# Optimization experiments

Hardware: AMD Instinct MI355X
Metric: run time of the kernel (lower is better)

The kernel has to match this reference:

```python
import jax, jax.numpy as jnp
import numpy as np

DIM = 1024
HEADS = 16
HEAD_DIM = DIM // HEADS
WINDOW = 512
NEG = -1e9  # matches masked_fill(-1e9) semantics; excluded keys get ~0 weight


def setup_inputs() -> dict:
    key = jax.random.key(0)
    ks = jax.random.split(key, 9)
    s = 1.0 / np.sqrt(DIM)
    inp = {"x": jax.random.normal(ks[0], (2, 4096, DIM), dtype=jnp.float32)}
    for i, name in enumerate(["q", "k", "v", "o"]):
        inp[f"W{name}"] = jax.random.uniform(ks[1 + 2 * i], (DIM, DIM), jnp.float32, -s, s)
        inp[f"b{name}"] = jax.random.uniform(ks[2 + 2 * i], (DIM,), jnp.float32, -s, s)
    return inp


def _sliding_window_attn(x, Wq, bq, Wk, bk, Wv, bv, Wo, bo):
    B, S, D = x.shape
    H, hd, W = HEADS, HEAD_DIM, WINDOW
    nb = S // W  # number of query blocks

    def proj(Wp, bp):
        y = x @ Wp.T + bp                       # [B,S,D]
        return y.reshape(B, S, H, hd).transpose(0, 2, 1, 3)  # [B,H,S,hd]

    q = proj(Wq, bq)
    k = proj(Wk, bk)
    v = proj(Wv, bv)

    scale = hd ** -0.5
    qb = q.reshape(B, H, nb, W, hd)

    def window_kv(t):
        # each query block n attends to blocks n-1 and n (2W keys)
        pad = jnp.concatenate([jnp.zeros((B, H, W, hd), t.dtype), t], axis=2)
        prev = pad[:, :, :S].reshape(B, H, nb, W, hd)
        cur = t.reshape(B, H, nb, W, hd)
        return jnp.concatenate([prev, cur], axis=3)  # [B,H,nb,2W,hd]

    kw = window_kv(k)
    vw = window_kv(v)

    scores = jnp.einsum('bhnqd,bhnkd->bhnqk', qb, kw) * scale  # [B,H,nb,W,2W]

    # key abs pos = n*W - W + t ; query abs pos = n*W + s
    t = jnp.arange(2 * W)            # [2W]
    s_ = jnp.arange(W)[:, None]      # [W,1]
    n = jnp.arange(nb)[:, None, None]  # [nb,1,1]
    valid = (t <= s_ + W) & (t >= s_ + 1) & (n * W - W + t >= 0)  # [nb,W,2W]
    scores = jnp.where(valid, scores, NEG)

    attn = jax.nn.softmax(scores, axis=-1)
    out = jnp.einsum('bhnqk,bhnkd->bhnqd', attn, vw)  # [B,H,nb,W,hd]
    out = out.reshape(B, H, S, hd).transpose(0, 2, 1, 3).reshape(B, S, D)
    return out @ Wo.T + bo


def reference(x, Wq, bq, Wk, bk, Wv, bv, Wo, bo):
    return _sliding_window_attn(x, Wq, bq, Wk, bk, Wv, bv, Wo, bo)
```

## Files before the change

kernel.cpp:

```cpp
#include <hip/hip_runtime.h>
#include <hip/hip_bf16.h>

typedef __bf16 bf16_t;
typedef __attribute__((ext_vector_type(8))) __bf16 bfrag;
typedef __attribute__((ext_vector_type(4))) float f32x4;

#define SEQ    4096
#define NDIM   1024
#define NHEAD  16
#define HD     64
#define NBATCH 2
#define MROWS  (NBATCH * SEQ)
#define LQKV   3072

__device__ __forceinline__ void gload_lds16(const bf16_t* g, bf16_t* l) {
    __builtin_amdgcn_global_load_lds(
        (const __attribute__((address_space(1))) unsigned int*)g,
        (__attribute__((address_space(3))) unsigned int*)l,
        16, 0, 0);
}

#define DPPF(v, ctrl) __builtin_bit_cast(float, \
    __builtin_amdgcn_update_dpp(0, __builtin_bit_cast(int, (v)), (ctrl), 0xF, 0xF, true))

__device__ __forceinline__ float rowmax16(float v) {
    v = fmaxf(v, DPPF(v, 0xB1));
    v = fmaxf(v, DPPF(v, 0x4E));
    v = fmaxf(v, DPPF(v, 0x141));
    v = fmaxf(v, DPPF(v, 0x140));
    return v;
}
__device__ __forceinline__ float rowsum16(float v) {
    v += DPPF(v, 0xB1);
    v += DPPF(v, 0x4E);
    v += DPPF(v, 0x141);
    v += DPPF(v, 0x140);
    return v;
}

template <typename OT>
__global__ __launch_bounds__(256, 2)
void gemm_bt(const bf16_t* __restrict__ A, int lda,
             const bf16_t* __restrict__ W,
             const float* __restrict__ b0p, const float* __restrict__ b1p,
             const float* __restrict__ b2p,
             OT* __restrict__ C, int ldc, int K)
{
    __shared__ __align__(16) bf16_t As[128 * 32];
    __shared__ __align__(16) bf16_t Bs[128 * 32];

    const int tid  = threadIdx.x;
    const int lane = tid & 63;
    const int wid  = tid >> 6;
    const int n16  = lane & 15;
    const int quad = lane >> 4;
    const int row0 = blockIdx.y * 128;
    const int col0 = blockIdx.x * 128;
    const int wrow = (wid >> 1) * 64;
    const int wcol = (wid & 1) * 64;
    const float* bias = (col0 < 1024) ? b0p : (col0 < 2048 ? b1p : b2p);
    const int bcol0 = col0 & 1023;

    f32x4 acc[4][4];
#pragma unroll
    for (int i = 0; i < 4; i++)
#pragma unroll
        for (int j = 0; j < 4; j++) acc[i][j] = (f32x4){0.f, 0.f, 0.f, 0.f};

    for (int k0 = 0; k0 < K; k0 += 32) {
#pragma unroll
        for (int it = 0; it < 2; it++) {
            int idx = tid + it * 256;
            int r   = idx >> 2;
            int c   = (idx & 3) * 8;
            gload_lds16(A + (size_t)(row0 + r) * lda + k0 + c, &As[(it * 256 + wid * 64) * 8]);
            gload_lds16(W + (size_t)(col0 + r) * K   + k0 + c, &Bs[(it * 256 + wid * 64) * 8]);
        }
        __syncthreads();

        bfrag af[4], bfg[4];
#pragma unroll
        for (int i = 0; i < 4; i++)
            af[i] = *(const bfrag*)(&As[(wrow + i * 16 + n16) * 32 + quad * 8]);
#pragma unroll
        for (int j = 0; j < 4; j++)
            bfg[j] = *(const bfrag*)(&Bs[(wcol + j * 16 + n16) * 32 + quad * 8]);

#pragma unroll
        for (int i = 0; i < 4; i++)
#pragma unroll
            for (int j = 0; j < 4; j++)
                acc[i][j] = __builtin_amdgcn_mfma_f32_16x16x32_bf16(af[i], bfg[j], acc[i][j], 0, 0, 0);
        __syncthreads();
    }

#pragma unroll
    for (int i = 0; i < 4; i++) {
#pragma unroll
        for (int j = 0; j < 4; j++) {
#pragma unroll
            for (int r = 0; r < 4; r++) {
                int row = row0 + wrow + i * 16 + quad * 4 + r;
                int col = wcol + j * 16 + n16;
                float v = acc[i][j][r] + bias[bcol0 + col];
                C[(size_t)row * ldc + col0 + col] = (OT)v;
            }
        }
    }
}

__global__ __launch_bounds__(256)
void cast_x(const float* __restrict__ s, bf16_t* __restrict__ d)
{
    size_t i = ((size_t)blockIdx.x * 256 + threadIdx.x) * 8;
    float4 a = *(const float4*)(s + i);
    float4 b = *(const float4*)(s + i + 4);
    bfrag o;
    o[0] = (__bf16)a.x; o[1] = (__bf16)a.y; o[2] = (__bf16)a.z; o[3] = (__bf16)a.w;
    o[4] = (__bf16)b.x; o[5] = (__bf16)b.y; o[6] = (__bf16)b.z; o[7] = (__bf16)b.w;
    *(bfrag*)(d + i) = o;
}

__global__ __launch_bounds__(256)
void cast_w(const float* __restrict__ wq, const float* __restrict__ wk,
            const float* __restrict__ wv, const float* __restrict__ wo,
            bf16_t* __restrict__ d)
{
    size_t t   = (size_t)blockIdx.x * 256 + threadIdx.x;
    int    sel = (int)(t >> 17);
    const float* s = sel == 0 ? wq : (sel == 1 ? wk : (sel == 2 ? wv : wo));
    size_t off = (t & 131071) * 8;
    float4 a = *(const float4*)(s + off);
    float4 b = *(const float4*)(s + off + 4);
    bfrag o;
    o[0] = (__bf16)a.x; o[1] = (__bf16)a.y; o[2] = (__bf16)a.z; o[3] = (__bf16)a.w;
    o[4] = (__bf16)b.x; o[5] = (__bf16)b.y; o[6] = (__bf16)b.z; o[7] = (__bf16)b.w;
    *(bfrag*)(d + (size_t)sel * 1048576 + off) = o;
}

__global__ __launch_bounds__(256, 2)
void vtrans(const bf16_t* __restrict__ QKV, bf16_t* __restrict__ Vt)
{
    __shared__ __align__(16) bf16_t T[64 * 72];
    const int tid = threadIdx.x;
    const int s0  = blockIdx.x * 64;
    const int bh  = blockIdx.y;
    const int b   = bh >> 4, h = bh & 15;
    const size_t bS   = (size_t)b * SEQ;
    const size_t hoff = (size_t)h * HD;

#pragma unroll
    for (int u = 0; u < 2; u++) {
        int idx = tid + u * 256;
        int t = idx >> 3, c = (idx & 7) * 8;
        *(uint4*)&T[t * 72 + c] =
            *(const uint4*)&QKV[(bS + s0 + t) * LQKV + 2048 + hoff + c];
    }
    __syncthreads();
#pragma unroll
    for (int u = 0; u < 2; u++) {
        int idx = tid + u * 256;
        int d = idx >> 3, t8 = (idx & 7) * 8;
        bfrag v;
#pragma unroll
        for (int e = 0; e < 8; e++) v[e] = T[(t8 + e) * 72 + d];
        *(bfrag*)&Vt[((size_t)bh * HD + d) * SEQ + s0 + t8] = v;
    }
}

__global__ __launch_bounds__(256, 4)
void attn_win(const bf16_t* __restrict__ QKV, const bf16_t* __restrict__ Vt,
              bf16_t* __restrict__ AO)
{
    __shared__ __align__(16) bf16_t Ks[2][64 * 72];
    __shared__ __align__(16) bf16_t Pw[4][16 * 72];

    const int tid  = threadIdx.x;
    const int wid  = tid >> 6;
    const int lane = tid & 63;
    const int n16  = lane & 15;
    const int quad = lane >> 4;

    const int q0 = blockIdx.x * 64;
    const int bh = blockIdx.y;
    const int b  = bh >> 4, h = bh & 15;
    const size_t bS   = (size_t)b * SEQ;
    const size_t hoff = (size_t)h * HD;
    const bf16_t* Vb  = Vt + (size_t)bh * HD * SEQ;
    const int wstart  = q0 - 512;
    const int it0     = (q0 < 512) ? ((512 - q0) >> 6) : 0;

    const int srow  = tid >> 2;
    const int scol0 = (tid & 3) * 16;

    const int mq = wid * 16 + n16;
    bfrag aq0 = *(const bfrag*)(&QKV[(bS + q0 + mq) * LQKV + hoff + quad * 8]);
    bfrag aq1 = *(const bfrag*)(&QKV[(bS + q0 + mq) * LQKV + hoff + 32 + quad * 8]);

    f32x4 ao[4];
#pragma unroll
    for (int j = 0; j < 4; j++) ao[j] = (f32x4){0.f, 0.f, 0.f, 0.f};
    float m[4] = {-1e30f, -1e30f, -1e30f, -1e30f};
    float l[4] = {0.f, 0.f, 0.f, 0.f};

    uint4 kp0, kp1;
    {
        const bf16_t* src = &QKV[(bS + wstart + it0 * 64 + srow) * LQKV + 1024 + hoff + scol0];
        kp0 = *(const uint4*)(src);
        kp1 = *(const uint4*)(src + 8);
    }

    for (int it = it0; it < 9; ++it) {
        const int pb = it & 1;
        *(uint4*)(&Ks[pb][srow * 72 + scol0])     = kp0;
        *(uint4*)(&Ks[pb][srow * 72 + scol0 + 8]) = kp1;
        __syncthreads();
        if (it < 8) {
            const bf16_t* src = &QKV[(bS + wstart + (it + 1) * 64 + srow) * LQKV + 1024 + hoff + scol0];
            kp0 = *(const uint4*)(src);
            kp1 = *(const uint4*)(src + 8);
        }

        f32x4 a[4];
#pragma unroll
        for (int nt = 0; nt < 4; nt++) {
            bfrag b0 = *(const bfrag*)(&Ks[pb][(nt * 16 + n16) * 72 + quad * 8]);
            bfrag b1 = *(const bfrag*)(&Ks[pb][(nt * 16 + n16) * 72 + 32 + quad * 8]);
            f32x4 s4 = (f32x4){0.f, 0.f, 0.f, 0.f};
            s4 = __builtin_amdgcn_mfma_f32_16x16x32_bf16(aq0, b0, s4, 0, 0, 0);
            s4 = __builtin_amdgcn_mfma_f32_16x16x32_bf16(aq1, b1, s4, 0, 0, 0);
            a[nt] = s4;
        }

        const bool msk = (it == 0) || (it == 8);
        if (msk) {
#pragma unroll
            for (int nt = 0; nt < 4; nt++)
#pragma unroll
                for (int r = 0; r < 4; r++) {
                    int ka = wstart + it * 64 + nt * 16 + n16;
                    int qa = q0 + wid * 16 + quad * 4 + r;
                    bool valid = (ka >= qa - 511) & (ka <= qa);
                    a[nt][r] = valid ? a[nt][r] * 0.125f : -1e30f;
                }
        } else {
#pragma unroll
            for (int nt = 0; nt < 4; nt++)
#pragma unroll
                for (int r = 0; r < 4; r++) a[nt][r] *= 0.125f;
        }

        float alpha[4];
#pragma unroll
        for (int r = 0; r < 4; r++) {
            float cm = fmaxf(fmaxf(a[0][r], a[1][r]), fmaxf(a[2][r], a[3][r]));
            cm = rowmax16(cm);
            float mn = fmaxf(m[r], cm);
            alpha[r] = __expf(m[r] - mn);
            m[r] = mn;
        }
#pragma unroll
        for (int j = 0; j < 4; j++)
#pragma unroll
            for (int r = 0; r < 4; r++) ao[j][r] *= alpha[r];

        float lacc[4] = {0.f, 0.f, 0.f, 0.f};
#pragma unroll
        for (int nt = 0; nt < 4; nt++) {
#pragma unroll
            for (int r = 0; r < 4; r++) {
                float p;
                if (msk) p = (a[nt][r] > -1e29f) ? __expf(a[nt][r] - m[r]) : 0.f;
                else     p = __expf(a[nt][r] - m[r]);
                lacc[r] += p;
                Pw[wid][(quad * 4 + r) * 72 + nt * 16 + n16] = (bf16_t)p;
            }
        }
#pragma unroll
        for (int r = 0; r < 4; r++) l[r] = l[r] * alpha[r] + lacc[r];

#pragma unroll
        for (int ks = 0; ks < 2; ks++) {
            bfrag ap = *(const bfrag*)(&Pw[wid][n16 * 72 + ks * 32 + quad * 8]);
#pragma unroll
            for (int j = 0; j < 4; j++) {
                bfrag bv = *(const bfrag*)(&Vb[(size_t)(j * 16 + n16) * SEQ
                                               + wstart + it * 64 + ks * 32 + quad * 8]);
                ao[j] = __builtin_amdgcn_mfma_f32_16x16x32_bf16(ap, bv, ao[j], 0, 0, 0);
            }
        }
    }

    float inv[4];
#pragma unroll
    for (int r = 0; r < 4; r++) inv[r] = 1.0f / rowsum16(l[r]);
#pragma unroll
    for (int j = 0; j < 4; j++)
#pragma unroll
        for (int r = 0; r < 4; r++) {
            int qa = q0 + wid * 16 + quad * 4 + r;
            AO[(bS + qa) * NDIM + hoff + j * 16 + n16] = (bf16_t)(ao[j][r] * inv[r]);
        }
}

extern "C" void kernel_launch(void* const* d_in, const int* in_sizes, int n_in,
                              void* d_out, int out_size, void* d_ws, size_t ws_size,
                              hipStream_t stream)
{
    const float* x  = (const float*)d_in[0];
    const float* Wq = (const float*)d_in[1];
    const float* bq = (const float*)d_in[2];
    const float* Wk = (const float*)d_in[3];
    const float* bk = (const float*)d_in[4];
    const float* Wv = (const float*)d_in[5];
    const float* bv = (const float*)d_in[6];
    const float* Wo = (const float*)d_in[7];
    const float* bo = (const float*)d_in[8];
    float* out = (float*)d_out;

    const size_t QKV_E = (size_t)MROWS * LQKV;
    const size_t X_E   = (size_t)MROWS * NDIM;
    if (ws_size < (QKV_E + X_E + 4u * 1048576u) * sizeof(bf16_t)) return;

    bf16_t* QKVb = (bf16_t*)d_ws;
    bf16_t* AbX  = QKVb + QKV_E;
    bf16_t* Wc   = AbX + X_E;
    bf16_t* Wob  = Wc + 3u * 1048576u;
    bf16_t* Vtg  = (bf16_t*)d_out;

    dim3 blk(256);

    cast_x<<<dim3(4096), blk, 0, stream>>>(x, AbX);
    cast_w<<<dim3(2048), blk, 0, stream>>>(Wq, Wk, Wv, Wo, Wc);

    gemm_bt<bf16_t><<<dim3(LQKV / 128, MROWS / 128), blk, 0, stream>>>(
        AbX, NDIM, Wc, bq, bk, bv, QKVb, LQKV, NDIM);

    vtrans<<<dim3(SEQ / 64, NBATCH * NHEAD), blk, 0, stream>>>(QKVb, Vtg);

    attn_win<<<dim3(SEQ / 64, NBATCH * NHEAD), blk, 0, stream>>>(QKVb, Vtg, AbX);

    gemm_bt<float><<<dim3(NDIM / 128, MROWS / 128), blk, 0, stream>>>(
        AbX, NDIM, Wob, bo, bo, bo, out, NDIM, NDIM);
}
```

Before: 291.8 us.

## Fuse V transpose into QKV GEMM epilogue and transpose attention MFMA orientation

The QKV GEMM epilogue now writes the V columns straight into a transposed per-head layout, which removes the separate vtrans kernel and the V slice of the QKV buffer. The attention kernel computes S^T (keys as rows), so each lane owns one query column. Softmax reductions then use two cross-quad shuffles instead of DPP row reductions, and P and output stores become packed 4-wide. K tiles are now read directly from global memory instead of being staged through double-buffered LDS, which drops the block barriers but relies on caches for K reuse across waves.

```diff
diff --git a/kernel.cpp b/kernel.cpp
--- a/kernel.cpp
+++ b/kernel.cpp
@@ -3,6 +3,7 @@
 
 typedef __bf16 bf16_t;
 typedef __attribute__((ext_vector_type(8))) __bf16 bfrag;
+typedef __attribute__((ext_vector_type(4))) __bf16 bf16x4;
 typedef __attribute__((ext_vector_type(4))) float f32x4;
 
 #define SEQ    4096
@@ -11,31 +12,14 @@
 #define HD     64
 #define NBATCH 2
 #define MROWS  (NBATCH * SEQ)
-#define LQKV   3072
+#define LQK    2048
+#define PSTR   76
 
 __device__ __forceinline__ void gload_lds16(const bf16_t* g, bf16_t* l) {
     __builtin_amdgcn_global_load_lds(
         (const __attribute__((address_space(1))) unsigned int*)g,
         (__attribute__((address_space(3))) unsigned int*)l,
         16, 0, 0);
-}
-
-#define DPPF(v, ctrl) __builtin_bit_cast(float, \
-    __builtin_amdgcn_update_dpp(0, __builtin_bit_cast(int, (v)), (ctrl), 0xF, 0xF, true))
-
-__device__ __forceinline__ float rowmax16(float v) {
-    v = fmaxf(v, DPPF(v, 0xB1));
-    v = fmaxf(v, DPPF(v, 0x4E));
-    v = fmaxf(v, DPPF(v, 0x141));
-    v = fmaxf(v, DPPF(v, 0x140));
-    return v;
-}
-__device__ __forceinline__ float rowsum16(float v) {
-    v += DPPF(v, 0xB1);
-    v += DPPF(v, 0x4E);
-    v += DPPF(v, 0x141);
-    v += DPPF(v, 0x140);
-    return v;
 }
 
 template <typename OT>
@@ -44,7 +28,8 @@
              const bf16_t* __restrict__ W,
              const float* __restrict__ b0p, const float* __restrict__ b1p,
              const float* __restrict__ b2p,
-             OT* __restrict__ C, int ldc, int K)
+             OT* __restrict__ C, int ldc, int K,
+             bf16_t* __restrict__ VtOut)
 {
     __shared__ __align__(16) bf16_t As[128 * 32];
     __shared__ __align__(16) bf16_t Bs[128 * 32];
@@ -94,16 +79,32 @@
         __syncthreads();
     }
 
-#pragma unroll
-    for (int i = 0; i < 4; i++) {
-#pragma unroll
-        for (int j = 0; j < 4; j++) {
-#pragma unroll
-            for (int r = 0; r < 4; r++) {
-                int row = row0 + wrow + i * 16 + quad * 4 + r;
-                int col = wcol + j * 16 + n16;
-                float v = acc[i][j][r] + bias[bcol0 + col];
-                C[(size_t)row * ldc + col0 + col] = (OT)v;
+    if (col0 < 2048 || VtOut == nullptr) {
+#pragma unroll
+        for (int i = 0; i < 4; i++)
+#pragma unroll
+            for (int j = 0; j < 4; j++)
+#pragma unroll
+                for (int r = 0; r < 4; r++) {
+                    int row = row0 + wrow + i * 16 + quad * 4 + r;
+                    int col = wcol + j * 16 + n16;
+                    float v = acc[i][j][r] + bias[bcol0 + col];
+                    C[(size_t)row * ldc + col0 + col] = (OT)v;
+                }
+    } else {
+#pragma unroll
+        for (int i = 0; i < 4; i++) {
+#pragma unroll
+            for (int j = 0; j < 4; j++) {
+                int dg     = col0 + wcol + j * 16 + n16 - 2048;
+                int token0 = row0 + wrow + i * 16 + quad * 4;
+                int bb     = token0 >> 12;
+                float bv   = bias[bcol0 + wcol + j * 16 + n16];
+                size_t vrow = ((size_t)bb * NHEAD + (dg >> 6)) * HD + (dg & 63);
+                bf16x4 pk;
+#pragma unroll
+                for (int r = 0; r < 4; r++) pk[r] = (__bf16)(acc[i][j][r] + bv);
+                *(bf16x4*)&VtOut[vrow * SEQ + (token0 & (SEQ - 1))] = pk;
             }
         }
     }
@@ -138,42 +139,11 @@
     *(bfrag*)(d + (size_t)sel * 1048576 + off) = o;
 }
 
-__global__ __launch_bounds__(256, 2)
-void vtrans(const bf16_t* __restrict__ QKV, bf16_t* __restrict__ Vt)
-{
-    __shared__ __align__(16) bf16_t T[64 * 72];
-    const int tid = threadIdx.x;
-    const int s0  = blockIdx.x * 64;
-    const int bh  = blockIdx.y;
-    const int b   = bh >> 4, h = bh & 15;
-    const size_t bS   = (size_t)b * SEQ;
-    const size_t hoff = (size_t)h * HD;
-
-#pragma unroll
-    for (int u = 0; u < 2; u++) {
-        int idx = tid + u * 256;
-        int t = idx >> 3, c = (idx & 7) * 8;
-        *(uint4*)&T[t * 72 + c] =
-            *(const uint4*)&QKV[(bS + s0 + t) * LQKV + 2048 + hoff + c];
-    }
-    __syncthreads();
-#pragma unroll
-    for (int u = 0; u < 2; u++) {
-        int idx = tid + u * 256;
-        int d = idx >> 3, t8 = (idx & 7) * 8;
-        bfrag v;
-#pragma unroll
-        for (int e = 0; e < 8; e++) v[e] = T[(t8 + e) * 72 + d];
-        *(bfrag*)&Vt[((size_t)bh * HD + d) * SEQ + s0 + t8] = v;
-    }
-}
-
 __global__ __launch_bounds__(256, 4)
-void attn_win(const bf16_t* __restrict__ QKV, const bf16_t* __restrict__ Vt,
+void attn_win(const bf16_t* __restrict__ QK, const bf16_t* __restrict__ Vt,
               bf16_t* __restrict__ AO)
 {
-    __shared__ __align__(16) bf16_t Ks[2][64 * 72];
-    __shared__ __align__(16) bf16_t Pw[4][16 * 72];
+    __shared__ __align__(16) bf16_t Pw[4][16 * PSTR];
 
     const int tid  = threadIdx.x;
     const int wid  = tid >> 6;
@@ -190,45 +160,27 @@
     const int wstart  = q0 - 512;
     const int it0     = (q0 < 512) ? ((512 - q0) >> 6) : 0;
 
-    const int srow  = tid >> 2;
-    const int scol0 = (tid & 3) * 16;
-
-    const int mq = wid * 16 + n16;
-    bfrag aq0 = *(const bfrag*)(&QKV[(bS + q0 + mq) * LQKV + hoff + quad * 8]);
-    bfrag aq1 = *(const bfrag*)(&QKV[(bS + q0 + mq) * LQKV + hoff + 32 + quad * 8]);
+    const int qa = q0 + wid * 16 + n16;
+    bfrag bq0 = *(const bfrag*)(&QK[(bS + qa) * LQK + hoff + quad * 8]);
+    bfrag bq1 = *(const bfrag*)(&QK[(bS + qa) * LQK + hoff + 32 + quad * 8]);
 
     f32x4 ao[4];
 #pragma unroll
     for (int j = 0; j < 4; j++) ao[j] = (f32x4){0.f, 0.f, 0.f, 0.f};
-    float m[4] = {-1e30f, -1e30f, -1e30f, -1e30f};
-    float l[4] = {0.f, 0.f, 0.f, 0.f};
-
-    uint4 kp0, kp1;
-    {
-        const bf16_t* src = &QKV[(bS + wstart + it0 * 64 + srow) * LQKV + 1024 + hoff + scol0];
-        kp0 = *(const uint4*)(src);
-        kp1 = *(const uint4*)(src + 8);
-    }
+    float m = -1e30f, l = 0.f;
 
     for (int it = it0; it < 9; ++it) {
-        const int pb = it & 1;
-        *(uint4*)(&Ks[pb][srow * 72 + scol0])     = kp0;
-        *(uint4*)(&Ks[pb][srow * 72 + scol0 + 8]) = kp1;
-        __syncthreads();
-        if (it < 8) {
-            const bf16_t* src = &QKV[(bS + wstart + (it + 1) * 64 + srow) * LQKV + 1024 + hoff + scol0];
-            kp0 = *(const uint4*)(src);
-            kp1 = *(const uint4*)(src + 8);
-        }
+        const int k0 = wstart + it * 64;
 
         f32x4 a[4];
 #pragma unroll
         for (int nt = 0; nt < 4; nt++) {
-            bfrag b0 = *(const bfrag*)(&Ks[pb][(nt * 16 + n16) * 72 + quad * 8]);
-            bfrag b1 = *(const bfrag*)(&Ks[pb][(nt * 16 + n16) * 72 + 32 + quad * 8]);
+            const bf16_t* krow = &QK[(bS + k0 + nt * 16 + n16) * LQK + 1024 + hoff];
+            bfrag ak0 = *(const bfrag*)(krow + quad * 8);
+            bfrag ak1 = *(const bfrag*)(krow + 32 + quad * 8);
             f32x4 s4 = (f32x4){0.f, 0.f, 0.f, 0.f};
-            s4 = __builtin_amdgcn_mfma_f32_16x16x32_bf16(aq0, b0, s4, 0, 0, 0);
-            s4 = __builtin_amdgcn_mfma_f32_16x16x32_bf16(aq1, b1, s4, 0, 0, 0);
+            s4 = __builtin_amdgcn_mfma_f32_16x16x32_bf16(ak0, bq0, s4, 0, 0, 0);
+            s4 = __builtin_amdgcn_mfma_f32_16x16x32_bf16(ak1, bq1, s4, 0, 0, 0);
             a[nt] = s4;
         }
 
@@ -238,8 +190,7 @@
             for (int nt = 0; nt < 4; nt++)
 #pragma unroll
                 for (int r = 0; r < 4; r++) {
-                    int ka = wstart + it * 64 + nt * 16 + n16;
-                    int qa = q0 + wid * 16 + quad * 4 + r;
+                    int ka = k0 + nt * 16 + quad * 4 + r;
                     bool valid = (ka >= qa - 511) & (ka <= qa);
                     a[nt][r] = valid ? a[nt][r] * 0.125f : -1e30f;
                 }
@@ -250,57 +201,58 @@
                 for (int r = 0; r < 4; r++) a[nt][r] *= 0.125f;
         }
 
-        float alpha[4];
-#pragma unroll
-        for (int r = 0; r < 4; r++) {
-            float cm = fmaxf(fmaxf(a[0][r], a[1][r]), fmaxf(a[2][r], a[3][r]));
-            cm = rowmax16(cm);
-            float mn = fmaxf(m[r], cm);
-            alpha[r] = __expf(m[r] - mn);
-            m[r] = mn;
-        }
+        float cm = -1e30f;
+#pragma unroll
+        for (int nt = 0; nt < 4; nt++)
+#pragma unroll
+            for (int r = 0; r < 4; r++) cm = fmaxf(cm, a[nt][r]);
+        cm = fmaxf(cm, __shfl_xor(cm, 16, 64));
+        cm = fmaxf(cm, __shfl_xor(cm, 32, 64));
+        float mn    = fmaxf(m, cm);
+        float alpha = __expf(m - mn);
+        m = mn;
 #pragma unroll
         for (int j = 0; j < 4; j++)
 #pragma unroll
-            for (int r = 0; r < 4; r++) ao[j][r] *= alpha[r];
-
-        float lacc[4] = {0.f, 0.f, 0.f, 0.f};
+            for (int r = 0; r < 4; r++) ao[j][r] *= alpha;
+
+        float lacc = 0.f;
 #pragma unroll
         for (int nt = 0; nt < 4; nt++) {
+            bf16x4 pk;
 #pragma unroll
             for (int r = 0; r < 4; r++) {
-                float p;
-                if (msk) p = (a[nt][r] > -1e29f) ? __expf(a[nt][r] - m[r]) : 0.f;
-                else     p = __expf(a[nt][r] - m[r]);
-                lacc[r] += p;
-                Pw[wid][(quad * 4 + r) * 72 + nt * 16 + n16] = (bf16_t)p;
+                float p = __expf(a[nt][r] - m);
+                if (msk && a[nt][r] <= -1e29f) p = 0.f;
+                lacc += p;
+                pk[r] = (__bf16)p;
             }
-        }
-#pragma unroll
-        for (int r = 0; r < 4; r++) l[r] = l[r] * alpha[r] + lacc[r];
+            *(bf16x4*)&Pw[wid][n16 * PSTR + nt * 16 + quad * 4] = pk;
+        }
+        l = l * alpha + lacc;
 
 #pragma unroll
         for (int ks = 0; ks < 2; ks++) {
-            bfrag ap = *(const bfrag*)(&Pw[wid][n16 * 72 + ks * 32 + quad * 8]);
+            bfrag bp = *(const bfrag*)(&Pw[wid][n16 * PSTR + ks * 32 + quad * 8]);
 #pragma unroll
             for (int j = 0; j < 4; j++) {
-                bfrag bv = *(const bfrag*)(&Vb[(size_t)(j * 16 + n16) * SEQ
-                                               + wstart + it * 64 + ks * 32 + quad * 8]);
-                ao[j] = __builtin_amdgcn_mfma_f32_16x16x32_bf16(ap, bv, ao[j], 0, 0, 0);
+                bfrag av = *(const bfrag*)(&Vb[(size_t)(j * 16 + n16) * SEQ
+                                               + k0 + ks * 32 + quad * 8]);
+                ao[j] = __builtin_amdgcn_mfma_f32_16x16x32_bf16(av, bp, ao[j], 0, 0, 0);
             }
         }
     }
 
-    float inv[4];
-#pragma unroll
-    for (int r = 0; r < 4; r++) inv[r] = 1.0f / rowsum16(l[r]);
-#pragma unroll
-    for (int j = 0; j < 4; j++)
-#pragma unroll
-        for (int r = 0; r < 4; r++) {
-            int qa = q0 + wid * 16 + quad * 4 + r;
-            AO[(bS + qa) * NDIM + hoff + j * 16 + n16] = (bf16_t)(ao[j][r] * inv[r]);
-        }
+    l += __shfl_xor(l, 16, 64);
+    l += __shfl_xor(l, 32, 64);
+    const float inv = 1.0f / l;
+#pragma unroll
+    for (int j = 0; j < 4; j++) {
+        bf16x4 pk;
+#pragma unroll
+        for (int r = 0; r < 4; r++) pk[r] = (__bf16)(ao[j][r] * inv);
+        *(bf16x4*)&AO[(bS + qa) * NDIM + hoff + j * 16 + quad * 4] = pk;
+    }
 }
 
 extern "C" void kernel_launch(void* const* d_in, const int* in_sizes, int n_in,
@@ -318,28 +270,26 @@
     const float* bo = (const float*)d_in[8];
     float* out = (float*)d_out;
 
-    const size_t QKV_E = (size_t)MROWS * LQKV;
-    const size_t X_E   = (size_t)MROWS * NDIM;
-    if (ws_size < (QKV_E + X_E + 4u * 1048576u) * sizeof(bf16_t)) return;
-
-    bf16_t* QKVb = (bf16_t*)d_ws;
-    bf16_t* AbX  = QKVb + QKV_E;
-    bf16_t* Wc   = AbX + X_E;
-    bf16_t* Wob  = Wc + 3u * 1048576u;
-    bf16_t* Vtg  = (bf16_t*)d_out;
+    const size_t QK_E = (size_t)MROWS * LQK;
+    const size_t X_E  = (size_t)MROWS * NDIM;
+    if (ws_size < (QK_E + X_E + 4u * 1048576u) * sizeof(bf16_t)) return;
+
+    bf16_t* QKb = (bf16_t*)d_ws;
+    bf16_t* AbX = QKb + QK_E;
+    bf16_t* Wc  = AbX + X_E;
+    bf16_t* Wob = Wc + 3u * 1048576u;
+    bf16_t* Vtg = (bf16_t*)d_out;
 
     dim3 blk(256);
 
     cast_x<<<dim3(4096), blk, 0, stream>>>(x, AbX);
     cast_w<<<dim3(2048), blk, 0, stream>>>(Wq, Wk, Wv, Wo, Wc);
 
-    gemm_bt<bf16_t><<<dim3(LQKV / 128, MROWS / 128), blk, 0, stream>>>(
-        AbX, NDIM, Wc, bq, bk, bv, QKVb, LQKV, NDIM);
-
-    vtrans<<<dim3(SEQ / 64, NBATCH * NHEAD), blk, 0, stream>>>(QKVb, Vtg);
-
-    attn_win<<<dim3(SEQ / 64, NBATCH * NHEAD), blk, 0, stream>>>(QKVb, Vtg, AbX);
+    gemm_bt<bf16_t><<<dim3(3072 / 128, MROWS / 128), blk, 0, stream>>>(
+        AbX, NDIM, Wc, bq, bk, bv, QKb, LQK, NDIM, Vtg);
+
+    attn_win<<<dim3(SEQ / 64, NBATCH * NHEAD), blk, 0, stream>>>(QKb, Vtg, AbX);
 
     gemm_bt<float><<<dim3(NDIM / 128, MROWS / 128), blk, 0, stream>>>(
-        AbX, NDIM, Wob, bo, bo, bo, out, NDIM, NDIM);
-}
+        AbX, NDIM, Wob, bo, bo, bo, out, NDIM, NDIM, nullptr);
+}
```

New measurement: 331.0 us. 1.13x slower.
